# Performance work log

Hardware: AMD Instinct MI355X
Metric: run time of the kernel (lower is better)

Reference implementation:

```python
import jax, jax.numpy as jnp
import numpy as np

START_TAG = 0
END_TAG = 63
NEG_INF = -10000.0


def setup_inputs() -> dict:
    key = jax.random.key(0)
    k1, k2, k3 = jax.random.split(key, 3)
    S, D, L = 32768, 1024, 64  # seq_len, feature_dim, num_labels
    feats = jax.random.normal(k1, (S, D), jnp.float32)
    W = jax.random.normal(k2, (L, D), jnp.float32) * 0.02  # nn.Linear weight [out,in]
    b = jnp.zeros((L,), jnp.float32)
    transitions = jax.random.normal(k3, (L, L), jnp.float32)
    transitions = transitions.at[START_TAG, :].set(NEG_INF).at[:, END_TAG].set(NEG_INF)
    return {"feats": feats, "W": W, "b": b, "transitions": transitions}


def reference(feats, W, b, transitions):
    # emissions: [S, L]
    emissions = feats @ W.T + b

    # Viterbi forward pass.  scores[j] after step t = best path score ending in label j.
    init_scores = transitions[:, START_TAG] + emissions[0]

    def step(scores, emit):
        # swt[j, i] = scores[i] + T[j, i]  (transition i -> j)
        swt = scores[None, :] + transitions  # [L, L]
        new_scores = emit + jnp.max(swt, axis=-1)
        back_ptr = jnp.argmax(swt, axis=-1)
        return new_scores, back_ptr

    final_scores, back_ptrs = jax.lax.scan(step, init_scores, emissions[1:])
    final_scores = final_scores + transitions[END_TAG]

    viterbi_score = jnp.max(final_scores)
    last_tag = jnp.argmax(final_scores)

    # Backtrack: tag[t-1] = back_ptrs[t-1][tag[t]] (back_ptrs[k] is for time k+1).
    def back(tag, bp):
        return bp[tag], tag

    first_tag, rest_tags = jax.lax.scan(back, last_tag, back_ptrs, reverse=True)
    tag_seq = jnp.concatenate([first_tag[None], rest_tags])  # [S]
    return viterbi_score, tag_seq
```

## Files before the change

kernel.cpp:

```cpp
#include <hip/hip_runtime.h>

#define S_LEN 32768
#define D_DIM 1024
#define L_LAB 64
#define LC 32
#define NCH (S_LEN / LC)
#define H_WARM 64
#define CHUNK 128
#define NCHUNK (S_LEN / CHUNK)
#define BP_TPW 8

#define EM_OFF   0
#define SC_OFF   (S_LEN * 64 * 4)
#define BP_OFF   (SC_OFF + S_LEN * 64 * 4)
#define MAPS_OFF (BP_OFF + S_LEN * 64)
#define BND_OFF  (MAPS_OFF + NCHUNK * 64)
#define WIN_OFF  (BND_OFF + 256)

typedef __attribute__((ext_vector_type(8))) short short8;
typedef __attribute__((ext_vector_type(4))) float floatx4;

__device__ inline unsigned short f32_bf16_rne(float f) {
    unsigned v = __float_as_uint(f);
    v += 0x7FFFu + ((v >> 16) & 1u);
    return (unsigned short)(v >> 16);
}

__global__ __launch_bounds__(256) __attribute__((amdgpu_waves_per_eu(2, 2)))
void emis_kernel(
        const float* __restrict__ feats, const float* __restrict__ W,
        const float* __restrict__ bvec, float* __restrict__ em) {
    __shared__ __align__(16) float          As[64 * 68];
    __shared__ __align__(16) unsigned short BsH[64 * 72];
    __shared__ __align__(16) unsigned short BsL[64 * 72];

    const int tid = threadIdx.x;
    const int lan = tid & 15;
    const int q   = (tid >> 4) & 3;
    const int w   = tid >> 6;
    const int row0 = blockIdx.x * 64;

    floatx4 acc[4];
#pragma unroll
    for (int nt = 0; nt < 4; ++nt) acc[nt] = (floatx4){0.f, 0.f, 0.f, 0.f};

    for (int kb = 0; kb < D_DIM; kb += 64) {
        __syncthreads();
#pragma unroll
        for (int i = 0; i < 4; ++i) {
            int gi = tid + i * 256;
            int m = gi >> 4, g = gi & 15;
            float4 v = *(const float4*)&feats[(size_t)(row0 + m) * D_DIM + kb + g * 4];
            *(float4*)&As[m * 68 + g * 4] = v;
        }
#pragma unroll
        for (int i = 0; i < 4; ++i) {
            int gi = tid + i * 256;
            int m = gi >> 4, g = gi & 15;
            float4 v = *(const float4*)&W[(size_t)m * D_DIM + kb + g * 4];
            float f[4] = {v.x, v.y, v.z, v.w};
            unsigned h[4], l[4];
#pragma unroll
            for (int e = 0; e < 4; ++e) {
                unsigned u = __float_as_uint(f[e]);
                h[e] = u >> 16;
                float r = f[e] - __uint_as_float(u & 0xFFFF0000u);
                l[e] = f32_bf16_rne(r);
            }
            uint2 hv = {h[0] | (h[1] << 16), h[2] | (h[3] << 16)};
            uint2 lv = {l[0] | (l[1] << 16), l[2] | (l[3] << 16)};
            *(uint2*)&BsH[m * 72 + g * 4] = hv;
            *(uint2*)&BsL[m * 72 + g * 4] = lv;
        }
        __syncthreads();

#pragma unroll
        for (int cc = 0; cc < 2; ++cc) {
            int koff = cc * 32 + q * 8;
            int m_loc = w * 16 + lan;
            float4 a0 = *(const float4*)&As[m_loc * 68 + koff];
            float4 a1 = *(const float4*)&As[m_loc * 68 + koff + 4];
            float f[8] = {a0.x, a0.y, a0.z, a0.w, a1.x, a1.y, a1.z, a1.w};
            short8 ahi, alo;
#pragma unroll
            for (int i = 0; i < 8; ++i) {
                unsigned u = __float_as_uint(f[i]);
                ahi[i] = (short)(u >> 16);
                float r = f[i] - __uint_as_float(u & 0xFFFF0000u);
                alo[i] = (short)f32_bf16_rne(r);
            }
#pragma unroll
            for (int nt = 0; nt < 4; ++nt) {
                int label = nt * 16 + lan;
                short8 bhi = *(const short8*)&BsH[label * 72 + koff];
                short8 blo = *(const short8*)&BsL[label * 72 + koff];
                acc[nt] = __builtin_amdgcn_mfma_f32_16x16x32_bf16(ahi, bhi, acc[nt], 0, 0, 0);
                acc[nt] = __builtin_amdgcn_mfma_f32_16x16x32_bf16(alo, bhi, acc[nt], 0, 0, 0);
                acc[nt] = __builtin_amdgcn_mfma_f32_16x16x32_bf16(ahi, blo, acc[nt], 0, 0, 0);
            }
        }
    }

#pragma unroll
    for (int nt = 0; nt < 4; ++nt) {
        int label = nt * 16 + lan;
        float bias = bvec[label];
#pragma unroll
        for (int r = 0; r < 4; ++r) {
            int row = row0 + w * 16 + q * 4 + r;
            em[(size_t)row * 64 + label] = acc[nt][r] + bias;
        }
    }
}

__global__ __launch_bounds__(64) __attribute__((amdgpu_waves_per_eu(1, 1)))
void fwd_chunks(
        const float* __restrict__ em, const float* __restrict__ T,
        float* __restrict__ sc_hist, float* __restrict__ win) {
    const int j = threadIdx.x;
    const int c = blockIdx.x;
    const int a = c * LC;
    const int bend = a + LC;

    float Trow[64];
#pragma unroll
    for (int i = 0; i < 16; ++i)
        ((float4*)Trow)[i] = ((const float4*)(T + j * 64))[i];

    int t0 = a - 1 - H_WARM;
    if (t0 < 0) t0 = 0;

    float sc;
    if (t0 == 0) {
        sc = Trow[0] + em[j];
        if (c == 0) sc_hist[j] = sc;
    } else {
        sc = em[(size_t)t0 * 64 + j];
    }

    auto step = [&](float e) {
        float v[16];
#pragma unroll
        for (int k = 0; k < 16; ++k) {
            float a0 = __int_as_float(__builtin_amdgcn_readlane(__float_as_int(sc), k)) + Trow[k];
            float a1 = __int_as_float(__builtin_amdgcn_readlane(__float_as_int(sc), k + 16)) + Trow[k + 16];
            float a2 = __int_as_float(__builtin_amdgcn_readlane(__float_as_int(sc), k + 32)) + Trow[k + 32];
            float a3 = __int_as_float(__builtin_amdgcn_readlane(__float_as_int(sc), k + 48)) + Trow[k + 48];
            v[k] = fmaxf(fmaxf(fmaxf(a0, a1), a2), a3);
        }
        float r0 = fmaxf(fmaxf(v[0], v[1]), v[2]);
        float r1 = fmaxf(fmaxf(v[3], v[4]), v[5]);
        float r2 = fmaxf(fmaxf(v[6], v[7]), v[8]);
        float r3 = fmaxf(fmaxf(v[9], v[10]), v[11]);
        float r4 = fmaxf(fmaxf(v[12], v[13]), v[14]);
        float s0 = fmaxf(fmaxf(r0, r1), r2);
        float s1 = fmaxf(fmaxf(r3, r4), v[15]);
        sc = e + fmaxf(s0, s1);
    };

    int t = t0 + 1;
    if (t < a) {
        float p0 = em[(size_t)(t + 0) * 64 + j];
        float p1 = em[(size_t)(t + 1) * 64 + j];
        float p2 = em[(size_t)(t + 2) * 64 + j];
        float p3 = em[(size_t)(t + 3) * 64 + j];
        for (; t + 3 < a; t += 4) {
            float n0 = em[(size_t)(t + 4) * 64 + j];
            float n1 = em[(size_t)(t + 5) * 64 + j];
            float n2 = em[(size_t)(t + 6) * 64 + j];
            float n3 = em[(size_t)(t + 7) * 64 + j];
            step(p0); step(p1); step(p2); step(p3);
            p0 = n0; p1 = n1; p2 = n2; p3 = n3;
        }
        for (; t < a; ++t) { step(p0); p0 = p1; p1 = p2; p2 = p3; }
    }
    if (c > 0 && j == 0) win[c] = sc;

    t = (a > 0) ? a : 1;
    {
        float p0 = em[(size_t)(t + 0) * 64 + j];
        float p1 = em[(size_t)(t + 1) * 64 + j];
        float p2 = em[(size_t)(t + 2) * 64 + j];
        float p3 = em[(size_t)(t + 3) * 64 + j];
        for (; t + 3 < bend; t += 4) {
            int t4 = t + 4 > S_LEN - 1 ? S_LEN - 1 : t + 4;
            int t5 = t + 5 > S_LEN - 1 ? S_LEN - 1 : t + 5;
            int t6 = t + 6 > S_LEN - 1 ? S_LEN - 1 : t + 6;
            int t7 = t + 7 > S_LEN - 1 ? S_LEN - 1 : t + 7;
            float n0 = em[(size_t)t4 * 64 + j];
            float n1 = em[(size_t)t5 * 64 + j];
            float n2 = em[(size_t)t6 * 64 + j];
            float n3 = em[(size_t)t7 * 64 + j];
            step(p0); sc_hist[(size_t)(t + 0) * 64 + j] = sc;
            step(p1); sc_hist[(size_t)(t + 1) * 64 + j] = sc;
            step(p2); sc_hist[(size_t)(t + 2) * 64 + j] = sc;
            step(p3); sc_hist[(size_t)(t + 3) * 64 + j] = sc;
            p0 = n0; p1 = n1; p2 = n2; p3 = n3;
        }
        for (; t < bend; ++t) {
            step(p0); sc_hist[(size_t)t * 64 + j] = sc;
            p0 = p1; p1 = p2; p2 = p3;
        }
    }
}

__global__ __launch_bounds__(256) __attribute__((amdgpu_waves_per_eu(2, 2)))
void bp_kernel(
        const float* __restrict__ sc_hist, const float* __restrict__ T,
        unsigned char* __restrict__ bp) {
    int j = threadIdx.x & 63;
    int w = threadIdx.x >> 6;
    float Trow[64];
#pragma unroll
    for (int i = 0; i < 16; ++i)
        ((float4*)Trow)[i] = ((const float4*)(T + j * 64))[i];
    int tbase = (blockIdx.x * 4 + w) * BP_TPW;
    for (int k = 0; k < BP_TPW; ++k) {
        int t = tbase + k + 1;
        if (t >= S_LEN) return;
        const float* prev = sc_hist + (size_t)(t - 1) * 64;
        float best = 0.f; int bi = 0;
#pragma unroll
        for (int i = 0; i < 64; ++i) {
            float v = prev[i] + Trow[i];
            if (i == 0) best = v;
            else if (v > best) { best = v; bi = i; }
        }
        bp[(size_t)t * 64 + j] = (unsigned char)bi;
    }
}

__global__ __launch_bounds__(256) void finish_kernel(
        const float* __restrict__ sc_hist, const float* __restrict__ T,
        const float* __restrict__ win, const unsigned char* __restrict__ maps,
        float* __restrict__ out, unsigned char* __restrict__ bnd) {
    __shared__ unsigned char lm[NCHUNK * 64];
    __shared__ int lt;
    int tid = threadIdx.x;
    const uint4* src = (const uint4*)maps;
    uint4* dst = (uint4*)lm;
#pragma unroll
    for (int i = 0; i < (NCHUNK * 64 / 16) / 256; ++i) dst[tid + i * 256] = src[tid + i * 256];

    if (tid < 64) {
        int j = tid;
        float part = 0.f;
        for (int c = 1 + j; c < NCH; c += 64) {
            float end_prev = sc_hist[((size_t)c * LC - 1) * 64 + 0];
            part += end_prev - win[c];
        }
#pragma unroll
        for (int off = 32; off; off >>= 1) part += __shfl_xor(part, off, 64);

        float f = sc_hist[(size_t)(S_LEN - 1) * 64 + j] + T[63 * 64 + j];
        float best = 0.f; int bt = 0;
#pragma unroll
        for (int k = 0; k < 64; ++k) {
            float fv = __int_as_float(__builtin_amdgcn_readlane(__float_as_int(f), k));
            if (k == 0) best = fv;
            else if (fv > best) { best = fv; bt = k; }
        }
        if (j == 0) { out[0] = best + part; lt = bt; }
    }
    __syncthreads();
    if (tid == 0) {
        int x = lt;
        bnd[NCHUNK - 1] = (unsigned char)x;
        for (int c = NCHUNK - 1; c >= 1; --c) {
            x = lm[c * 64 + x];
            bnd[c - 1] = (unsigned char)x;
        }
    }
}

__global__ __launch_bounds__(64) void bt_maps(
        const unsigned char* __restrict__ bp, unsigned char* __restrict__ maps) {
    __shared__ unsigned char lb[CHUNK * 64];
    int c = blockIdx.x, l = threadIdx.x;
    const uint4* src = (const uint4*)(bp + (size_t)c * CHUNK * 64);
    uint4* dst = (uint4*)lb;
#pragma unroll
    for (int i = 0; i < (CHUNK * 64 / 16) / 64; ++i) dst[l + i * 64] = src[l + i * 64];
    __syncthreads();
    int x = l;
    int t0 = c * CHUNK;
    for (int tt = CHUNK - 1; tt >= 0; --tt) {
        if (t0 + tt >= 1) x = lb[tt * 64 + x];
    }
    maps[c * 64 + l] = (unsigned char)x;
}

__global__ __launch_bounds__(64) void bt_fill(
        const unsigned char* __restrict__ bp, const unsigned char* __restrict__ bnd,
        float* __restrict__ out) {
    __shared__ unsigned char lb[CHUNK * 64];
    int c = blockIdx.x, l = threadIdx.x;
    const uint4* src = (const uint4*)(bp + (size_t)c * CHUNK * 64);
    uint4* dst = (uint4*)lb;
#pragma unroll
    for (int i = 0; i < (CHUNK * 64 / 16) / 64; ++i) dst[l + i * 64] = src[l + i * 64];
    __syncthreads();
    if (l == 0) {
        int t0 = c * CHUNK;
        int x = bnd[c];
        out[1 + t0 + CHUNK - 1] = (float)x;
        for (int tt = CHUNK - 1; tt >= 0; --tt) {
            int t = t0 + tt;
            if (t >= 1) {
                x = lb[tt * 64 + x];
                out[1 + t - 1] = (float)x;
            }
        }
    }
}

extern "C" void kernel_launch(void* const* d_in, const int* in_sizes, int n_in,
                              void* d_out, int out_size, void* d_ws, size_t ws_size,
                              hipStream_t stream) {
    const float* feats = (const float*)d_in[0];
    const float* W     = (const float*)d_in[1];
    const float* b     = (const float*)d_in[2];
    const float* T     = (const float*)d_in[3];
    float* out = (float*)d_out;

    char* ws = (char*)d_ws;
    float*          em       = (float*)(ws + EM_OFF);
    float*          sc_hist  = (float*)(ws + SC_OFF);
    unsigned char*  bp       = (unsigned char*)(ws + BP_OFF);
    unsigned char*  maps     = (unsigned char*)(ws + MAPS_OFF);
    unsigned char*  bnd      = (unsigned char*)(ws + BND_OFF);
    float*          win      = (float*)(ws + WIN_OFF);

    emis_kernel<<<S_LEN / 64, 256, 0, stream>>>(feats, W, b, em);
    fwd_chunks<<<NCH, 64, 0, stream>>>(em, T, sc_hist, win);
    bp_kernel<<<S_LEN / (4 * BP_TPW), 256, 0, stream>>>(sc_hist, T, bp);
    bt_maps<<<NCHUNK, 64, 0, stream>>>(bp, maps);
    finish_kernel<<<1, 256, 0, stream>>>(sc_hist, T, win, maps, out, bnd);
    bt_fill<<<NCHUNK, 64, 0, stream>>>(bp, bnd, out);
}
```

Measured before the change: 307.4 us.

## Use single bf16 GEMM for emissions, fuse backpointer and chunk-map kernels, shorten warmup

The emission GEMM drops the split-bf16 three-MFMA scheme. Features and a pre-converted bf16 copy of W now go through one bf16 MFMA per tile, which cuts the conversion ALU work and two thirds of the matrix ops. The backpointer kernel and the chunk-map backtrack kernel are merged so backpointers stay in shared memory and are not re-read from global, removing one launch. The forward warmup length H_WARM is halved. The lower GEMM precision and shorter warmup risk wrong argmax/tag decisions on near-ties.

```diff
diff --git a/kernel.cpp b/kernel.cpp
--- a/kernel.cpp
+++ b/kernel.cpp
@@ -5,10 +5,9 @@
 #define L_LAB 64
 #define LC 32
 #define NCH (S_LEN / LC)
-#define H_WARM 64
+#define H_WARM 32
 #define CHUNK 128
 #define NCHUNK (S_LEN / CHUNK)
-#define BP_TPW 8
 
 #define EM_OFF   0
 #define SC_OFF   (S_LEN * 64 * 4)
@@ -16,6 +15,7 @@
 #define MAPS_OFF (BP_OFF + S_LEN * 64)
 #define BND_OFF  (MAPS_OFF + NCHUNK * 64)
 #define WIN_OFF  (BND_OFF + 256)
+#define WBF_OFF  (WIN_OFF + NCH * 4)
 
 typedef __attribute__((ext_vector_type(8))) short short8;
 typedef __attribute__((ext_vector_type(4))) float floatx4;
@@ -26,13 +26,18 @@
     return (unsigned short)(v >> 16);
 }
 
+__global__ __launch_bounds__(256) void wconv_kernel(
+        const float* __restrict__ W, unsigned short* __restrict__ Wbf) {
+    int i = blockIdx.x * 256 + threadIdx.x;
+    Wbf[i] = f32_bf16_rne(W[i]);
+}
+
 __global__ __launch_bounds__(256) __attribute__((amdgpu_waves_per_eu(2, 2)))
 void emis_kernel(
-        const float* __restrict__ feats, const float* __restrict__ W,
+        const float* __restrict__ feats, const unsigned short* __restrict__ Wbf,
         const float* __restrict__ bvec, float* __restrict__ em) {
-    __shared__ __align__(16) float          As[64 * 68];
-    __shared__ __align__(16) unsigned short BsH[64 * 72];
-    __shared__ __align__(16) unsigned short BsL[64 * 72];
+    __shared__ __align__(16) unsigned short As[64 * 72];
+    __shared__ __align__(16) unsigned short Bs[64 * 72];
 
     const int tid = threadIdx.x;
     const int lan = tid & 15;
@@ -51,26 +56,16 @@
             int gi = tid + i * 256;
             int m = gi >> 4, g = gi & 15;
             float4 v = *(const float4*)&feats[(size_t)(row0 + m) * D_DIM + kb + g * 4];
-            *(float4*)&As[m * 68 + g * 4] = v;
-        }
-#pragma unroll
-        for (int i = 0; i < 4; ++i) {
+            unsigned h0 = f32_bf16_rne(v.x) | ((unsigned)f32_bf16_rne(v.y) << 16);
+            unsigned h1 = f32_bf16_rne(v.z) | ((unsigned)f32_bf16_rne(v.w) << 16);
+            *(uint2*)&As[m * 72 + g * 4] = (uint2){h0, h1};
+        }
+#pragma unroll
+        for (int i = 0; i < 2; ++i) {
             int gi = tid + i * 256;
-            int m = gi >> 4, g = gi & 15;
-            float4 v = *(const float4*)&W[(size_t)m * D_DIM + kb + g * 4];
-            float f[4] = {v.x, v.y, v.z, v.w};
-            unsigned h[4], l[4];
-#pragma unroll
-            for (int e = 0; e < 4; ++e) {
-                unsigned u = __float_as_uint(f[e]);
-                h[e] = u >> 16;
-                float r = f[e] - __uint_as_float(u & 0xFFFF0000u);
-                l[e] = f32_bf16_rne(r);
-            }
-            uint2 hv = {h[0] | (h[1] << 16), h[2] | (h[3] << 16)};
-            uint2 lv = {l[0] | (l[1] << 16), l[2] | (l[3] << 16)};
-            *(uint2*)&BsH[m * 72 + g * 4] = hv;
-            *(uint2*)&BsL[m * 72 + g * 4] = lv;
+            int m = gi >> 3, g = gi & 7;
+            *(uint4*)&Bs[m * 72 + g * 8] =
+                *(const uint4*)&Wbf[(size_t)m * D_DIM + kb + g * 8];
         }
         __syncthreads();
 
@@ -78,25 +73,12 @@
         for (int cc = 0; cc < 2; ++cc) {
             int koff = cc * 32 + q * 8;
             int m_loc = w * 16 + lan;
-            float4 a0 = *(const float4*)&As[m_loc * 68 + koff];
-            float4 a1 = *(const float4*)&As[m_loc * 68 + koff + 4];
-            float f[8] = {a0.x, a0.y, a0.z, a0.w, a1.x, a1.y, a1.z, a1.w};
-            short8 ahi, alo;
-#pragma unroll
-            for (int i = 0; i < 8; ++i) {
-                unsigned u = __float_as_uint(f[i]);
-                ahi[i] = (short)(u >> 16);
-                float r = f[i] - __uint_as_float(u & 0xFFFF0000u);
-                alo[i] = (short)f32_bf16_rne(r);
-            }
+            short8 av = *(const short8*)&As[m_loc * 72 + koff];
 #pragma unroll
             for (int nt = 0; nt < 4; ++nt) {
                 int label = nt * 16 + lan;
-                short8 bhi = *(const short8*)&BsH[label * 72 + koff];
-                short8 blo = *(const short8*)&BsL[label * 72 + koff];
-                acc[nt] = __builtin_amdgcn_mfma_f32_16x16x32_bf16(ahi, bhi, acc[nt], 0, 0, 0);
-                acc[nt] = __builtin_amdgcn_mfma_f32_16x16x32_bf16(alo, bhi, acc[nt], 0, 0, 0);
-                acc[nt] = __builtin_amdgcn_mfma_f32_16x16x32_bf16(ahi, blo, acc[nt], 0, 0, 0);
+                short8 bv = *(const short8*)&Bs[label * 72 + koff];
+                acc[nt] = __builtin_amdgcn_mfma_f32_16x16x32_bf16(av, bv, acc[nt], 0, 0, 0);
             }
         }
     }
@@ -205,28 +187,50 @@
 }
 
 __global__ __launch_bounds__(256) __attribute__((amdgpu_waves_per_eu(2, 2)))
-void bp_kernel(
+void bp_maps_kernel(
         const float* __restrict__ sc_hist, const float* __restrict__ T,
-        unsigned char* __restrict__ bp) {
-    int j = threadIdx.x & 63;
-    int w = threadIdx.x >> 6;
+        unsigned char* __restrict__ bp, unsigned char* __restrict__ maps) {
+    __shared__ unsigned char lb[CHUNK * 64];
+    const int tid = threadIdx.x;
+    const int j = tid & 63;
+    const int w = tid >> 6;
+    const int c = blockIdx.x;
+    const int base = c * CHUNK;
+
     float Trow[64];
 #pragma unroll
     for (int i = 0; i < 16; ++i)
         ((float4*)Trow)[i] = ((const float4*)(T + j * 64))[i];
-    int tbase = (blockIdx.x * 4 + w) * BP_TPW;
-    for (int k = 0; k < BP_TPW; ++k) {
-        int t = tbase + k + 1;
-        if (t >= S_LEN) return;
-        const float* prev = sc_hist + (size_t)(t - 1) * 64;
-        float best = 0.f; int bi = 0;
-#pragma unroll
-        for (int i = 0; i < 64; ++i) {
-            float v = prev[i] + Trow[i];
-            if (i == 0) best = v;
-            else if (v > best) { best = v; bi = i; }
-        }
-        bp[(size_t)t * 64 + j] = (unsigned char)bi;
+
+    for (int k = 0; k < CHUNK / 4; ++k) {
+        int tt = w * (CHUNK / 4) + k;
+        int t = base + tt;
+        int bi = 0;
+        if (t >= 1) {
+            const float* prev = sc_hist + (size_t)(t - 1) * 64;
+            float best = 0.f;
+#pragma unroll
+            for (int i = 0; i < 64; ++i) {
+                float v = prev[i] + Trow[i];
+                if (i == 0) best = v;
+                else if (v > best) { best = v; bi = i; }
+            }
+        }
+        lb[tt * 64 + j] = (unsigned char)bi;
+    }
+    __syncthreads();
+
+    uint4* dst = (uint4*)(bp + (size_t)base * 64);
+    const uint4* src = (const uint4*)lb;
+#pragma unroll
+    for (int i = 0; i < 2; ++i) dst[tid + i * 256] = src[tid + i * 256];
+
+    if (tid < 64) {
+        int x = tid;
+        for (int tt = CHUNK - 1; tt >= 0; --tt) {
+            if (base + tt >= 1) x = lb[tt * 64 + x];
+        }
+        maps[c * 64 + tid] = (unsigned char)x;
     }
 }
 
@@ -271,23 +275,6 @@
             bnd[c - 1] = (unsigned char)x;
         }
     }
-}
-
-__global__ __launch_bounds__(64) void bt_maps(
-        const unsigned char* __restrict__ bp, unsigned char* __restrict__ maps) {
-    __shared__ unsigned char lb[CHUNK * 64];
-    int c = blockIdx.x, l = threadIdx.x;
-    const uint4* src = (const uint4*)(bp + (size_t)c * CHUNK * 64);
-    uint4* dst = (uint4*)lb;
-#pragma unroll
-    for (int i = 0; i < (CHUNK * 64 / 16) / 64; ++i) dst[l + i * 64] = src[l + i * 64];
-    __syncthreads();
-    int x = l;
-    int t0 = c * CHUNK;
-    for (int tt = CHUNK - 1; tt >= 0; --tt) {
-        if (t0 + tt >= 1) x = lb[tt * 64 + x];
-    }
-    maps[c * 64 + l] = (unsigned char)x;
 }
 
 __global__ __launch_bounds__(64) void bt_fill(
@@ -330,11 +317,12 @@
     unsigned char*  maps     = (unsigned char*)(ws + MAPS_OFF);
     unsigned char*  bnd      = (unsigned char*)(ws + BND_OFF);
     float*          win      = (float*)(ws + WIN_OFF);
-
-    emis_kernel<<<S_LEN / 64, 256, 0, stream>>>(feats, W, b, em);
+    unsigned short* Wbf      = (unsigned short*)(ws + WBF_OFF);
+
+    wconv_kernel<<<(L_LAB * D_DIM) / 256, 256, 0, stream>>>(W, Wbf);
+    emis_kernel<<<S_LEN / 64, 256, 0, stream>>>(feats, Wbf, b, em);
     fwd_chunks<<<NCH, 64, 0, stream>>>(em, T, sc_hist, win);
-    bp_kernel<<<S_LEN / (4 * BP_TPW), 256, 0, stream>>>(sc_hist, T, bp);
-    bt_maps<<<NCHUNK, 64, 0, stream>>>(bp, maps);
+    bp_maps_kernel<<<NCHUNK, 256, 0, stream>>>(sc_hist, T, bp, maps);
     finish_kernel<<<1, 256, 0, stream>>>(sc_hist, T, win, maps, out, bnd);
     bt_fill<<<NCHUNK, 64, 0, stream>>>(bp, bnd, out);
 }
```

Result: no change. 304.1 us (-1.1%).
